# Performance work log

Hardware: AMD Instinct MI355X
Metric: run time of the kernel (lower is better)

## Reference

```python
import jax, jax.numpy as jnp
import numpy as np

B, TXT_T, MEL_T, N_MEL = 32, 256, 1600, 40
PAD_MAG = 1.0e12


def setup_inputs() -> dict:
    key = jax.random.key(0)
    k1, k2, k3, k4 = jax.random.split(key, 4)
    mu_logvar = jax.random.normal(k1, (B, TXT_T, 2 * N_MEL), jnp.float32)
    z = jax.random.normal(k2, (B, N_MEL, MEL_T), jnp.float32)
    text_lengths = jax.random.randint(k3, (B,), TXT_T // 2, TXT_T + 1).astype(jnp.int32)
    mel_lengths = jax.random.randint(k4, (B,), MEL_T // 2, MEL_T + 1).astype(jnp.int32)
    return {"mu_logvar": mu_logvar, "z": z,
            "text_lengths": text_lengths, "mel_lengths": mel_lengths}


def _mdn_log_prob(mu_logvar, z):
    # mu_logvar: [B, L, 2C], z: [B, C, T] -> log_prob_matrix [B, L, T]
    C = z.shape[1]
    mu, logvar = jnp.split(mu_logvar, 2, axis=-1)          # [B, L, C] each
    invvar = jnp.exp(-logvar)                               # [B, L, C]
    # mean_c((z - mu)^2 * invvar) expanded via matmuls (no [B,L,T,C] tensor)
    t1 = jnp.einsum('bct,blc->blt', z * z, invvar)
    t2 = jnp.einsum('bct,blc->blt', z, mu * invvar)
    t3 = jnp.sum(mu * mu * invvar, axis=-1)[:, :, None]
    mse = t1 - 2.0 * t2 + t3                                # [B, L, T]
    return -0.5 * (mse / C + jnp.mean(logvar, axis=-1)[:, :, None])


def _forward_dp(lp):
    # forward algorithm: log_alpha over (txt position, mel time) via scan over T
    Bb, L, T = lp.shape
    alpha0 = jnp.full((Bb, L + 1), -PAD_MAG, lp.dtype).at[:, 1].set(lp[:, 0, 0])

    def step(alpha, lp_t):
        stay = alpha[:, 1:] + 1e-7
        go = alpha[:, :-1] + 1e-7
        new = jnp.logaddexp(stay, go) + lp_t                # [B, L]
        alpha_new = jnp.concatenate(
            [jnp.full((Bb, 1), -PAD_MAG, lp.dtype), new], axis=1)
        return alpha_new, new

    _, ys = jax.lax.scan(step, alpha0, jnp.moveaxis(lp[:, :, 1:], 2, 0))
    log_alpha = jnp.concatenate([alpha0[:, 1:][None], ys], axis=0)  # [T, B, L]
    return log_alpha


def _viterbi(lp, text_lengths, mel_lengths):
    Bb, L, T = lp.shape
    beta0 = jnp.full((Bb, L), -PAD_MAG, lp.dtype).at[:, 0].set(lp[:, 0, 0])

    def fstep(beta, lp_t):
        shifted = jnp.concatenate(
            [jnp.full((Bb, 1), -PAD_MAG, lp.dtype), beta[:, :-1]], axis=1)
        new = jnp.maximum(beta, shifted) + lp_t
        return new, new

    _, ys = jax.lax.scan(fstep, beta0, jnp.moveaxis(lp[:, :, 1:], 2, 0))
    log_beta = jnp.transpose(jnp.concatenate([beta0[None], ys], axis=0), (1, 2, 0))  # [B, L, T]

    b_idx = jnp.arange(Bb)
    r0 = (text_lengths - 1).astype(jnp.float32)
    c0 = (mel_lengths - 1).astype(jnp.float32)

    def bstep(carry, _):
        rows, cols = carry
        ri = rows.astype(jnp.int32)
        ci = cols.astype(jnp.int32)
        # torch negative indexing wraps -> emulate with mod
        val_go = log_beta[b_idx, (ri - 1) % L, (ci - 1) % T]
        val_stay = log_beta[b_idx, ri % L, (ci - 1) % T]
        is_go = (val_go > val_stay).astype(rows.dtype)
        new_rows = jax.nn.relu(rows - is_go + 1.0) - 1.0
        new_cols = jax.nn.relu(cols) - 1.0
        return (new_rows, new_cols), new_rows

    _, path_ys = jax.lax.scan(bstep, (r0, c0), None, length=T - 1)
    full = jnp.concatenate([r0[None], path_ys], axis=0)     # [T, B], backward order
    path = full[::-1].T                                     # [B, T], chronological
    align = jax.nn.one_hot(path.astype(jnp.int32), L, dtype=lp.dtype)  # [B, T, L]

    def shift(a, ml):
        # F.pad(..., (-pad, pad)) on time axis: shift valid region to the front
        rolled = jnp.roll(a, -(T - ml), axis=0)
        mask = (jnp.arange(T) < ml)[:, None].astype(a.dtype)
        return rolled * mask

    return jax.vmap(shift)(align, mel_lengths)              # [B, T, L]


def reference(mu_logvar, z, text_lengths, mel_lengths):
    lp = _mdn_log_prob(mu_logvar, z)                        # [B, L, T]
    log_alpha = _forward_dp(lp)                             # [T, B, L]
    b_idx = jnp.arange(lp.shape[0])
    alpha_last = log_alpha[mel_lengths - 1, b_idx, text_lengths - 1]
    mdn_loss = -(alpha_last / mel_lengths.astype(alpha_last.dtype))  # [B]
    alignment = _viterbi(lp, text_lengths, mel_lengths)     # [B, T, L]
    return mdn_loss, alignment, lp
```

## Files before the change

### kernel.cpp

```cpp
#include <hip/hip_runtime.h>
#include <cstdint>
#include <math.h>

#define BB   32
#define LLEN 256
#define TLEN 1600
#define NC   40
#define NEGPADF (-1.0e12f)
#define NEGPADD (-1.0e12)
#define NBATCH 16
#define SUBB   8
#define NPROD  4
#define NBUF   2

#define LOG2E_F 1.4426950408889634f
#define LN2_F   0.6931471805599453f
#define C7F     1.4426950408889634e-7f

#define OFF_ALIGN 32
#define OFF_LP    (32 + (size_t)BB * TLEN * LLEN)

#define WSB_A    0
#define WSB_KC   (WSB_A + (size_t)BB * LLEN * 80 * 8)
#define WSB_LPT  (WSB_KC + (size_t)BB * LLEN * 8)

__device__ __forceinline__ int imin(int a, int b) { return a < b ? a : b; }

#define WAIT_LGKM0 0xC07F

__device__ __forceinline__ void bar_prod() {
  asm volatile("" ::: "memory");
  __builtin_amdgcn_s_waitcnt(WAIT_LGKM0);
  __builtin_amdgcn_s_barrier();
  asm volatile("" ::: "memory");
}
__device__ __forceinline__ void bar_cons() {
  asm volatile("" ::: "memory");
  __builtin_amdgcn_s_barrier();
  asm volatile("" ::: "memory");
}

__device__ __forceinline__ int rot1_i32(int x) {
  return __builtin_amdgcn_mov_dpp(x, 0x13C , 0xF, 0xF, true);
}
__device__ __forceinline__ float rot1_f32(float x) {
  return __int_as_float(rot1_i32(__float_as_int(x)));
}
__device__ __forceinline__ double rot1_f64(double x) {
  long long v = __double_as_longlong(x);
  int lo = rot1_i32((int)(v & 0xffffffffLL));
  int hi = rot1_i32((int)(v >> 32));
  return __longlong_as_double(((long long)hi << 32) | (unsigned long long)(unsigned int)lo);
}

__global__ __launch_bounds__(256) void prep_kernel(
    const float* __restrict__ mu_logvar, double* __restrict__ A, double* __restrict__ Kc) {
  int row = blockIdx.x * 4 + (threadIdx.x >> 6);
  int lane = threadIdx.x & 63;
  const float* src = mu_logvar + (size_t)row * (2 * NC);
  double mu = 0.0, lv = 0.0, iv = 0.0, part = 0.0;
  if (lane < NC) {
    mu = (double)src[lane];
    lv = (double)src[NC + lane];
    iv = exp(-lv);
    part = mu * mu * iv + lv;
  }
  for (int m = 1; m < 64; m <<= 1) part += __shfl_xor(part, m, 64);
  const double s = -0.5 / (double)NC;
  if (lane < NC) {
    A[(size_t)row * 80 + lane]      = s * iv;
    A[(size_t)row * 80 + NC + lane] = (1.0 / (double)NC) * mu * iv;
  }
  if (lane == 0) Kc[row] = s * part;
}

__global__ __launch_bounds__(128) void lp_kernel(
    const float* __restrict__ z, const double* __restrict__ A,
    const double* __restrict__ Kc, float* __restrict__ out,
    float* __restrict__ lpTh) {
  int b  = blockIdx.z;
  int l0 = blockIdx.y * 32;
  int t0 = blockIdx.x * 128;
  int tid = threadIdx.x;
  int t = t0 + tid;
  int tv = imin(t, TLEN - 1);
  bool act = (t < TLEN);

  float* lp_out = out + OFF_LP;
  float* loS    = out + OFF_ALIGN;

  float zr[NC];
  const float* zb = z + (size_t)b * NC * TLEN;
  #pragma unroll
  for (int c = 0; c < NC; ++c) zr[c] = zb[(size_t)c * TLEN + tv];

  __shared__ __align__(16) double tile[128][17];
  const double* Ab = A + ((size_t)b * LLEN + l0) * 80;
  const double* Kb = Kc + (size_t)b * LLEN + l0;

  for (int g = 0; g < 2; ++g) {
    for (int j16 = 0; j16 < 16; ++j16) {
      int j = g * 16 + j16;
      const double* Ar = Ab + (size_t)j * 80;
      double a0 = Kb[j], a1 = 0.0, a2 = 0.0, a3 = 0.0;
      #pragma unroll
      for (int c = 0; c < NC; c += 2) {
        double z0 = (double)zr[c], z1 = (double)zr[c + 1];
        a0 = fma(Ar[c],          z0 * z0, a0);
        a1 = fma(Ar[NC + c],     z0,      a1);
        a2 = fma(Ar[c + 1],      z1 * z1, a2);
        a3 = fma(Ar[NC + c + 1], z1,      a3);
      }
      double accd = (a0 + a2) + (a1 + a3);
      if (act) lp_out[((size_t)b * LLEN + l0 + j) * TLEN + t] = (float)accd;
      tile[tid][j16] = accd;
    }
    __syncthreads();
    #pragma unroll
    for (int p = 0; p < 4; ++p) {
      int idx = p * 128 + tid;
      int r = idx >> 2, c4 = idx & 3;
      int tr = t0 + r;
      if (tr < TLEN) {
        float h[4], lo[4];
        #pragma unroll
        for (int i = 0; i < 4; ++i) {
          double d = tile[r][c4 * 4 + i];
          float hh = (float)d;
          h[i] = hh;
          lo[i] = (float)(d - (double)hh);
        }
        size_t base = ((size_t)b * TLEN + tr) * LLEN + l0 + g * 16 + c4 * 4;
        *(float4*)(lpTh + base) = make_float4(h[0], h[1], h[2], h[3]);
        *(float4*)(loS + base)  = make_float4(lo[0], lo[1], lo[2], lo[3]);
      }
    }
    __syncthreads();
  }
}

__global__ __launch_bounds__(320, 1) void dp_kernel(
    const float* __restrict__ lpTh, const float* outR,
    const int* __restrict__ tlen, const int* __restrict__ mlen,
    float* __restrict__ out) {
  int bid = blockIdx.x;
  bool is_beta = (bid >= BB);
  int b = is_beta ? bid - BB : bid;
  int tid = threadIdx.x;
  int lane = tid & 63;
  int wv = tid >> 6;
  int tl = tlen[b];
  int ml = mlen[b];
  const float* lpb = lpTh + (size_t)b * TLEN * LLEN;
  const float* lob = outR + OFF_ALIGN + (size_t)b * TLEN * LLEN;
  float* al = out + OFF_ALIGN + (size_t)b * TLEN * LLEN;
  int nint = (ml - 2 + NBATCH) / NBATCH;

  __shared__ __align__(16) double bufd[NBUF][NBATCH][4][64];
  __shared__ uint32_t Dbits[LLEN][TLEN / 32];
  __shared__ int pathL[TLEN];
  float* bufaF = (float*)&bufd[0][0][0][0];

  if (wv >= 1) {
    int q = wv - 1;
    int nsb = 2 * nint;
    const float* ph = lpb + 4 * lane;
    const float* pl = lob + 4 * lane;
    float4 vh[SUBB], vl[SUBB];
    float4 z4 = make_float4(0.f, 0.f, 0.f, 0.f);
    auto issue = [&](int sb) {
      #pragma unroll
      for (int j = 0; j < SUBB; ++j) {
        int c = imin(1 + SUBB * sb + j, TLEN - 1);
        vh[j] = *(const float4*)(ph + (size_t)c * LLEN);
        if (is_beta) vl[j] = *(const float4*)(pl + (size_t)c * LLEN);
      }
    };
    auto store = [&](int sb) {
      int s  = (sb >> 1) % NBUF;
      int jb = (sb & 1) * SUBB;
      if (is_beta) {
        #pragma unroll
        for (int j = 0; j < SUBB; ++j) {
          bufd[s][jb + j][0][lane] = (double)vh[j].x + (double)vl[j].x;
          bufd[s][jb + j][1][lane] = (double)vh[j].y + (double)vl[j].y;
          bufd[s][jb + j][2][lane] = (double)vh[j].z + (double)vl[j].z;
          bufd[s][jb + j][3][lane] = (double)vh[j].w + (double)vl[j].w;
        }
      } else {
        #pragma unroll
        for (int j = 0; j < SUBB; ++j) {
          int off = ((s * NBATCH + jb + j) * 4) * 64 + lane;
          bufaF[off]       = fmaf(vh[j].x, LOG2E_F, C7F);
          bufaF[off + 64]  = fmaf(vh[j].y, LOG2E_F, C7F);
          bufaF[off + 128] = fmaf(vh[j].z, LOG2E_F, C7F);
          bufaF[off + 192] = fmaf(vh[j].w, LOG2E_F, C7F);
        }
      }
    };
    if (q < 2) {
      issue(q); store(q);
      if (q + NPROD < nsb) issue(q + NPROD);
    } else if (q < nsb) {
      issue(q);
    }
    for (int w = 0; w < nint; ++w) {
      bar_prod();
      int sb0 = 2 * w + 2;
      int mine = ((sb0 & 3) == q) ? sb0 : ((((sb0 + 1) & 3) == q) ? (sb0 + 1) : -1);
      if (mine >= 0 && mine < nsb) {
        store(mine);
        if (mine + NPROD < nsb) issue(mine + NPROD);
      }
      if (is_beta && w >= 1) {
        int zc = NBATCH * (w - 1) + 4 * q;
        float* az = al + (size_t)zc * LLEN + 4 * lane;
        #pragma unroll
        for (int k = 0; k < 4; ++k) *(float4*)(az + (size_t)k * LLEN) = z4;
      }
    }
    if (is_beta) {
      for (int c = NBATCH * (nint - 1) + q; c < TLEN; c += NPROD)
        *(float4*)(al + (size_t)c * LLEN + 4 * lane) = z4;
    }
  } else if (!is_beta) {
    float lp00 = lpb[0] * LOG2E_F;
    float o0 = (lane == 0) ? lp00 : NEGPADF;
    float o1 = NEGPADF, o2 = NEGPADF, o3 = NEGPADF;
    float f0 = o0, f1 = o1, f2 = o2, f3 = o3;
    float qv = rot1_f32(o3);
    int t = 1;
    for (int w = 0; w < nint; ++w) {
      bar_cons();
      int s = w % NBUF;
      #pragma unroll
      for (int j = 0; j < NBATCH; ++j, ++t) {
        int off = ((s * NBATCH + j) * 4) * 64 + lane;
        float l0 = bufaF[off];
        float l1 = bufaF[off + 64];
        float l2 = bufaF[off + 128];
        float l3 = bufaF[off + 192];
        float p = (lane == 0) ? NEGPADF : qv;
        float m0 = fmaxf(o0, p),  d0 = o0 - p;
        float m1 = fmaxf(o1, o0), d1 = o1 - o0;
        float m2 = fmaxf(o2, o1), d2 = o2 - o1;
        float m3 = fmaxf(o3, o2), d3 = o3 - o2;
        float n0 = m0 + __builtin_amdgcn_logf(1.0f + __builtin_amdgcn_exp2f(-fabsf(d0))) + l0;
        float n1 = m1 + __builtin_amdgcn_logf(1.0f + __builtin_amdgcn_exp2f(-fabsf(d1))) + l1;
        float n2 = m2 + __builtin_amdgcn_logf(1.0f + __builtin_amdgcn_exp2f(-fabsf(d2))) + l2;
        float n3 = m3 + __builtin_amdgcn_logf(1.0f + __builtin_amdgcn_exp2f(-fabsf(d3))) + l3;
        o0 = n0; o1 = n1; o2 = n2; o3 = n3;
        qv = rot1_f32(o3);
        if (t == ml - 1) { f0 = o0; f1 = o1; f2 = o2; f3 = o3; }
      }
    }
    int fr = tl - 1;
    if (lane == (fr >> 2)) {
      int sx = fr & 3;
      float val = (sx == 0) ? f0 : (sx == 1) ? f1 : (sx == 2) ? f2 : f3;
      out[b] = -val * LN2_F / (float)ml;
    }
  } else {
    double lp00 = (double)lpb[0] + (double)lob[0];
    double o0 = (lane == 0) ? lp00 : NEGPADD;
    double o1 = NEGPADD, o2 = NEGPADD, o3 = NEGPADD;
    uint32_t a0 = 0, a1 = (lane == 0) ? 1u : 0u, a2 = 0, a3 = 0;
    double qv = rot1_f64(o3);
    int t = 1;
    for (int w = 0; w < nint; ++w) {
      bar_cons();
      int s = w % NBUF;
      #pragma unroll
      for (int j = 0; j < NBATCH; ++j, ++t) {
        double l0 = bufd[s][j][0][lane];
        double l1 = bufd[s][j][1][lane];
        double l2 = bufd[s][j][2][lane];
        double l3 = bufd[s][j][3][lane];
        double p = (lane == 0) ? NEGPADD : qv;
        double n0 = fmax(o0, p)  + l0;
        double n1 = fmax(o1, o0) + l1;
        double n2 = fmax(o2, o1) + l2;
        double n3 = fmax(o3, o2) + l3;
        qv = rot1_f64(n3);
        uint32_t bit = 1u << (t & 31);
        if (qv > n0) a0 |= bit;
        if (n0 > n1) a1 |= bit;
        if (n1 > n2) a2 |= bit;
        if (n2 > n3) a3 |= bit;
        o0 = n0; o1 = n1; o2 = n2; o3 = n3;
        if ((t & 31) == 31) {
          int wd = t >> 5;
          Dbits[4 * lane + 0][wd] = a0; a0 = 0;
          Dbits[4 * lane + 1][wd] = a1; a1 = 0;
          Dbits[4 * lane + 2][wd] = a2; a2 = 0;
          Dbits[4 * lane + 3][wd] = a3; a3 = 0;
        }
      }
    }
    int tend = nint * NBATCH;
    int wd = tend >> 5;
    if ((tend & 31) != 31 && wd < TLEN / 32) {
      Dbits[4 * lane + 0][wd] = a0;
      Dbits[4 * lane + 1][wd] = a1;
      Dbits[4 * lane + 2][wd] = a2;
      Dbits[4 * lane + 3][wd] = a3;
    }
    __builtin_amdgcn_s_waitcnt(WAIT_LGKM0);

    if (lane == 0) {
      int r = tl - 1;
      pathL[ml - 1] = r;
      int curR = 1 << 30, curW = -1;
      uint32_t W = 0;
      for (int qq = ml - 2; qq >= 0; --qq) {
        int w2 = qq >> 5;
        if (r >= 0 && (r != curR || w2 != curW)) { W = Dbits[r][w2]; curR = r; curW = w2; }
        int g = (r >= 0) ? (int)((W >> (qq & 31)) & 1u) : 0;
        r -= g;
        pathL[qq] = r;
      }
    }
  }

  if (is_beta) {
    __syncthreads();
    for (int t = tid; t < ml; t += 320) {
      int p = pathL[t];
      if (p >= 0) al[(size_t)t * LLEN + p] = 1.0f;
    }
  }
}

extern "C" void kernel_launch(void* const* d_in, const int* in_sizes, int n_in,
                              void* d_out, int out_size, void* d_ws, size_t ws_size,
                              hipStream_t stream) {
  const float* mu_logvar = (const float*)d_in[0];
  const float* z         = (const float*)d_in[1];
  const int*   tlv       = (const int*)d_in[2];
  const int*   mlv       = (const int*)d_in[3];
  float* out = (float*)d_out;
  char*  wsb = (char*)d_ws;

  double* Ad   = (double*)(wsb + WSB_A);
  double* Kcd  = (double*)(wsb + WSB_KC);
  float*  lpTh = (float*)(wsb + WSB_LPT);

  prep_kernel<<<dim3(BB * LLEN / 4), 256, 0, stream>>>(mu_logvar, Ad, Kcd);
  lp_kernel<<<dim3(13, 8, BB), 128, 0, stream>>>(z, Ad, Kcd, out, lpTh);
  dp_kernel<<<dim3(2 * BB), 320, 0, stream>>>(lpTh, out, tlv, mlv, out);
}
```

Measured before the change: 516.0 us.

## Triple-buffer LDS staging and software-prefetch consumer loads four steps ahead

Raises the shared staging ring from two to three buffers and has producers fill one extra batch before the loop, so consumers can read into the next buffer early. Both the forward and Viterbi consumer loops now keep a 4-deep register ring of prefetched log-prob values, loading step j+4 while computing step j. This is meant to hide LDS load latency on the serial recurrence critical path. It costs more LDS and registers, especially in the f64 path, and needs an extra barrier so producer and consumer stay in lockstep.

```diff
diff --git a/kernel.cpp b/kernel.cpp
--- a/kernel.cpp
+++ b/kernel.cpp
@@ -11,7 +11,7 @@
 #define NBATCH 16
 #define SUBB   8
 #define NPROD  4
-#define NBUF   2
+#define NBUF   3
 
 #define LOG2E_F 1.4426950408889634f
 #define LN2_F   0.6931471805599453f
@@ -198,15 +198,14 @@
         }
       }
     };
-    if (q < 2) {
+    if (q < nsb) {
       issue(q); store(q);
       if (q + NPROD < nsb) issue(q + NPROD);
-    } else if (q < nsb) {
-      issue(q);
-    }
+    }
+    bar_prod();
     for (int w = 0; w < nint; ++w) {
       bar_prod();
-      int sb0 = 2 * w + 2;
+      int sb0 = 2 * w + 4;
       int mine = ((sb0 & 3) == q) ? sb0 : ((((sb0 + 1) & 3) == q) ? (sb0 + 1) : -1);
       if (mine >= 0 && mine < nsb) {
         store(mine);
@@ -229,17 +228,28 @@
     float o1 = NEGPADF, o2 = NEGPADF, o3 = NEGPADF;
     float f0 = o0, f1 = o1, f2 = o2, f3 = o3;
     float qv = rot1_f32(o3);
+    bar_cons();
+    float P[4][4];
+    #pragma unroll
+    for (int i = 0; i < 4; ++i) {
+      const float* src = bufaF + i * 256;
+      P[i][0] = src[lane]; P[i][1] = src[64 + lane];
+      P[i][2] = src[128 + lane]; P[i][3] = src[192 + lane];
+    }
     int t = 1;
     for (int w = 0; w < nint; ++w) {
       bar_cons();
-      int s = w % NBUF;
+      int s = w % NBUF, sn = (w + 1) % NBUF;
+      const float* baseS = bufaF + s * (NBATCH * 256);
+      const float* baseN = bufaF + sn * (NBATCH * 256);
       #pragma unroll
       for (int j = 0; j < NBATCH; ++j, ++t) {
-        int off = ((s * NBATCH + j) * 4) * 64 + lane;
-        float l0 = bufaF[off];
-        float l1 = bufaF[off + 64];
-        float l2 = bufaF[off + 128];
-        float l3 = bufaF[off + 192];
+        int rj = j & 3;
+        float l0 = P[rj][0], l1 = P[rj][1], l2 = P[rj][2], l3 = P[rj][3];
+        const float* src = (j < NBATCH - 4) ? (baseS + (j + 4) * 256)
+                                            : (baseN + (j + 4 - NBATCH) * 256);
+        P[rj][0] = src[lane];       P[rj][1] = src[64 + lane];
+        P[rj][2] = src[128 + lane]; P[rj][3] = src[192 + lane];
         float p = (lane == 0) ? NEGPADF : qv;
         float m0 = fmaxf(o0, p),  d0 = o0 - p;
         float m1 = fmaxf(o1, o0), d1 = o1 - o0;
@@ -266,16 +276,28 @@
     double o1 = NEGPADD, o2 = NEGPADD, o3 = NEGPADD;
     uint32_t a0 = 0, a1 = (lane == 0) ? 1u : 0u, a2 = 0, a3 = 0;
     double qv = rot1_f64(o3);
+    bar_cons();
+    double P[4][4];
+    #pragma unroll
+    for (int i = 0; i < 4; ++i) {
+      P[i][0] = bufd[0][i][0][lane]; P[i][1] = bufd[0][i][1][lane];
+      P[i][2] = bufd[0][i][2][lane]; P[i][3] = bufd[0][i][3][lane];
+    }
     int t = 1;
     for (int w = 0; w < nint; ++w) {
       bar_cons();
-      int s = w % NBUF;
+      int s = w % NBUF, sn = (w + 1) % NBUF;
+      const double (*bs)[4][64] = bufd[s];
+      const double (*bn)[4][64] = bufd[sn];
       #pragma unroll
       for (int j = 0; j < NBATCH; ++j, ++t) {
-        double l0 = bufd[s][j][0][lane];
-        double l1 = bufd[s][j][1][lane];
-        double l2 = bufd[s][j][2][lane];
-        double l3 = bufd[s][j][3][lane];
+        int rj = j & 3;
+        double l0 = P[rj][0], l1 = P[rj][1], l2 = P[rj][2], l3 = P[rj][3];
+        {
+          const double (*src)[64] = (j < NBATCH - 4) ? bs[j + 4] : bn[j + 4 - NBATCH];
+          P[rj][0] = src[0][lane]; P[rj][1] = src[1][lane];
+          P[rj][2] = src[2][lane]; P[rj][3] = src[3][lane];
+        }
         double p = (lane == 0) ? NEGPADD : qv;
         double n0 = fmax(o0, p)  + l0;
         double n1 = fmax(o1, o0) + l1;
```

New measurement: 489.6 us. 1.05x faster.

## Replace producer-wave LDS pipeline with single-wave register prefetch in DP kernel

Applied to the files above, without the earlier changes.

The DP kernel drops its four producer wavefronts, the double-buffered LDS staging and the per-batch block barriers. Each block is now one wavefront that prefetches the log-prob columns eight steps ahead into registers with a rotating set of float4 loads, and it zeroes the alignment rows inline. This removes barrier and LDS round-trip cost from the serial recurrence. The loop now runs over all TLEN steps instead of stopping at the mel length, and global load latency is hidden only by the eight-step prefetch depth.

```diff
diff --git a/kernel.cpp b/kernel.cpp
--- a/kernel.cpp
+++ b/kernel.cpp
@@ -8,10 +8,6 @@
 #define NC   40
 #define NEGPADF (-1.0e12f)
 #define NEGPADD (-1.0e12)
-#define NBATCH 16
-#define SUBB   8
-#define NPROD  4
-#define NBUF   2
 
 #define LOG2E_F 1.4426950408889634f
 #define LN2_F   0.6931471805599453f
@@ -27,18 +23,7 @@
 __device__ __forceinline__ int imin(int a, int b) { return a < b ? a : b; }
 
 #define WAIT_LGKM0 0xC07F
-
-__device__ __forceinline__ void bar_prod() {
-  asm volatile("" ::: "memory");
-  __builtin_amdgcn_s_waitcnt(WAIT_LGKM0);
-  __builtin_amdgcn_s_barrier();
-  asm volatile("" ::: "memory");
-}
-__device__ __forceinline__ void bar_cons() {
-  asm volatile("" ::: "memory");
-  __builtin_amdgcn_s_barrier();
-  asm volatile("" ::: "memory");
-}
+#define WAIT_VM0   0x3F70
 
 __device__ __forceinline__ int rot1_i32(int x) {
   return __builtin_amdgcn_mov_dpp(x, 0x13C , 0xF, 0xF, true);
@@ -139,120 +124,65 @@
   }
 }
 
-__global__ __launch_bounds__(320, 1) void dp_kernel(
+__global__ __launch_bounds__(64, 1) void dp_kernel(
     const float* __restrict__ lpTh, const float* outR,
     const int* __restrict__ tlen, const int* __restrict__ mlen,
-    float* __restrict__ out) {
+    float* out) {
   int bid = blockIdx.x;
   bool is_beta = (bid >= BB);
   int b = is_beta ? bid - BB : bid;
-  int tid = threadIdx.x;
-  int lane = tid & 63;
-  int wv = tid >> 6;
+  int lane = threadIdx.x & 63;
   int tl = tlen[b];
   int ml = mlen[b];
   const float* lpb = lpTh + (size_t)b * TLEN * LLEN;
   const float* lob = outR + OFF_ALIGN + (size_t)b * TLEN * LLEN;
   float* al = out + OFF_ALIGN + (size_t)b * TLEN * LLEN;
-  int nint = (ml - 2 + NBATCH) / NBATCH;
-
-  __shared__ __align__(16) double bufd[NBUF][NBATCH][4][64];
+
   __shared__ uint32_t Dbits[LLEN][TLEN / 32];
   __shared__ int pathL[TLEN];
-  float* bufaF = (float*)&bufd[0][0][0][0];
-
-  if (wv >= 1) {
-    int q = wv - 1;
-    int nsb = 2 * nint;
-    const float* ph = lpb + 4 * lane;
-    const float* pl = lob + 4 * lane;
-    float4 vh[SUBB], vl[SUBB];
-    float4 z4 = make_float4(0.f, 0.f, 0.f, 0.f);
-    auto issue = [&](int sb) {
-      #pragma unroll
-      for (int j = 0; j < SUBB; ++j) {
-        int c = imin(1 + SUBB * sb + j, TLEN - 1);
-        vh[j] = *(const float4*)(ph + (size_t)c * LLEN);
-        if (is_beta) vl[j] = *(const float4*)(pl + (size_t)c * LLEN);
-      }
-    };
-    auto store = [&](int sb) {
-      int s  = (sb >> 1) % NBUF;
-      int jb = (sb & 1) * SUBB;
-      if (is_beta) {
-        #pragma unroll
-        for (int j = 0; j < SUBB; ++j) {
-          bufd[s][jb + j][0][lane] = (double)vh[j].x + (double)vl[j].x;
-          bufd[s][jb + j][1][lane] = (double)vh[j].y + (double)vl[j].y;
-          bufd[s][jb + j][2][lane] = (double)vh[j].z + (double)vl[j].z;
-          bufd[s][jb + j][3][lane] = (double)vh[j].w + (double)vl[j].w;
-        }
-      } else {
-        #pragma unroll
-        for (int j = 0; j < SUBB; ++j) {
-          int off = ((s * NBATCH + jb + j) * 4) * 64 + lane;
-          bufaF[off]       = fmaf(vh[j].x, LOG2E_F, C7F);
-          bufaF[off + 64]  = fmaf(vh[j].y, LOG2E_F, C7F);
-          bufaF[off + 128] = fmaf(vh[j].z, LOG2E_F, C7F);
-          bufaF[off + 192] = fmaf(vh[j].w, LOG2E_F, C7F);
-        }
-      }
-    };
-    if (q < 2) {
-      issue(q); store(q);
-      if (q + NPROD < nsb) issue(q + NPROD);
-    } else if (q < nsb) {
-      issue(q);
-    }
-    for (int w = 0; w < nint; ++w) {
-      bar_prod();
-      int sb0 = 2 * w + 2;
-      int mine = ((sb0 & 3) == q) ? sb0 : ((((sb0 + 1) & 3) == q) ? (sb0 + 1) : -1);
-      if (mine >= 0 && mine < nsb) {
-        store(mine);
-        if (mine + NPROD < nsb) issue(mine + NPROD);
-      }
-      if (is_beta && w >= 1) {
-        int zc = NBATCH * (w - 1) + 4 * q;
-        float* az = al + (size_t)zc * LLEN + 4 * lane;
-        #pragma unroll
-        for (int k = 0; k < 4; ++k) *(float4*)(az + (size_t)k * LLEN) = z4;
-      }
-    }
-    if (is_beta) {
-      for (int c = NBATCH * (nint - 1) + q; c < TLEN; c += NPROD)
-        *(float4*)(al + (size_t)c * LLEN + 4 * lane) = z4;
-    }
-  } else if (!is_beta) {
+
+  const float* ph = lpb + 4 * lane;
+
+  if (!is_beta) {
     float lp00 = lpb[0] * LOG2E_F;
     float o0 = (lane == 0) ? lp00 : NEGPADF;
     float o1 = NEGPADF, o2 = NEGPADF, o3 = NEGPADF;
     float f0 = o0, f1 = o1, f2 = o2, f3 = o3;
     float qv = rot1_f32(o3);
+    float4 h0 = *(const float4*)(ph + 1 * LLEN);
+    float4 h1 = *(const float4*)(ph + 2 * LLEN);
+    float4 h2 = *(const float4*)(ph + 3 * LLEN);
+    float4 h3 = *(const float4*)(ph + 4 * LLEN);
+    float4 h4 = *(const float4*)(ph + 5 * LLEN);
+    float4 h5 = *(const float4*)(ph + 6 * LLEN);
+    float4 h6 = *(const float4*)(ph + 7 * LLEN);
+    float4 h7 = *(const float4*)(ph + 8 * LLEN);
     int t = 1;
-    for (int w = 0; w < nint; ++w) {
-      bar_cons();
-      int s = w % NBUF;
-      #pragma unroll
-      for (int j = 0; j < NBATCH; ++j, ++t) {
-        int off = ((s * NBATCH + j) * 4) * 64 + lane;
-        float l0 = bufaF[off];
-        float l1 = bufaF[off + 64];
-        float l2 = bufaF[off + 128];
-        float l3 = bufaF[off + 192];
-        float p = (lane == 0) ? NEGPADF : qv;
-        float m0 = fmaxf(o0, p),  d0 = o0 - p;
-        float m1 = fmaxf(o1, o0), d1 = o1 - o0;
-        float m2 = fmaxf(o2, o1), d2 = o2 - o1;
-        float m3 = fmaxf(o3, o2), d3 = o3 - o2;
-        float n0 = m0 + __builtin_amdgcn_logf(1.0f + __builtin_amdgcn_exp2f(-fabsf(d0))) + l0;
-        float n1 = m1 + __builtin_amdgcn_logf(1.0f + __builtin_amdgcn_exp2f(-fabsf(d1))) + l1;
-        float n2 = m2 + __builtin_amdgcn_logf(1.0f + __builtin_amdgcn_exp2f(-fabsf(d2))) + l2;
-        float n3 = m3 + __builtin_amdgcn_logf(1.0f + __builtin_amdgcn_exp2f(-fabsf(d3))) + l3;
-        o0 = n0; o1 = n1; o2 = n2; o3 = n3;
-        qv = rot1_f32(o3);
-        if (t == ml - 1) { f0 = o0; f1 = o1; f2 = o2; f3 = o3; }
-      }
+    auto stepA = [&](float4& hs) {
+      float4 hv = hs;
+      int c = imin(t + 8, TLEN - 1);
+      hs = *(const float4*)(ph + (size_t)c * LLEN);
+      float l0 = fmaf(hv.x, LOG2E_F, C7F);
+      float l1 = fmaf(hv.y, LOG2E_F, C7F);
+      float l2 = fmaf(hv.z, LOG2E_F, C7F);
+      float l3 = fmaf(hv.w, LOG2E_F, C7F);
+      float p = (lane == 0) ? NEGPADF : qv;
+      float m0 = fmaxf(o0, p),  d0 = o0 - p;
+      float m1 = fmaxf(o1, o0), d1 = o1 - o0;
+      float m2 = fmaxf(o2, o1), d2 = o2 - o1;
+      float m3 = fmaxf(o3, o2), d3 = o3 - o2;
+      float n0 = m0 + __builtin_amdgcn_logf(1.0f + __builtin_amdgcn_exp2f(-fabsf(d0))) + l0;
+      float n1 = m1 + __builtin_amdgcn_logf(1.0f + __builtin_amdgcn_exp2f(-fabsf(d1))) + l1;
+      float n2 = m2 + __builtin_amdgcn_logf(1.0f + __builtin_amdgcn_exp2f(-fabsf(d2))) + l2;
+      float n3 = m3 + __builtin_amdgcn_logf(1.0f + __builtin_amdgcn_exp2f(-fabsf(d3))) + l3;
+      o0 = n0; o1 = n1; o2 = n2; o3 = n3;
+      qv = rot1_f32(o3);
+      if (t == ml - 1) { f0 = o0; f1 = o1; f2 = o2; f3 = o3; }
+      ++t;
+    };
+    for (int tb = 0; tb < TLEN / 8; ++tb) {
+      stepA(h0); stepA(h1); stepA(h2); stepA(h3);
+      stepA(h4); stepA(h5); stepA(h6); stepA(h7);
     }
     int fr = tl - 1;
     if (lane == (fr >> 2)) {
@@ -260,74 +190,87 @@
       float val = (sx == 0) ? f0 : (sx == 1) ? f1 : (sx == 2) ? f2 : f3;
       out[b] = -val * LN2_F / (float)ml;
     }
-  } else {
-    double lp00 = (double)lpb[0] + (double)lob[0];
-    double o0 = (lane == 0) ? lp00 : NEGPADD;
-    double o1 = NEGPADD, o2 = NEGPADD, o3 = NEGPADD;
-    uint32_t a0 = 0, a1 = (lane == 0) ? 1u : 0u, a2 = 0, a3 = 0;
-    double qv = rot1_f64(o3);
-    int t = 1;
-    for (int w = 0; w < nint; ++w) {
-      bar_cons();
-      int s = w % NBUF;
-      #pragma unroll
-      for (int j = 0; j < NBATCH; ++j, ++t) {
-        double l0 = bufd[s][j][0][lane];
-        double l1 = bufd[s][j][1][lane];
-        double l2 = bufd[s][j][2][lane];
-        double l3 = bufd[s][j][3][lane];
-        double p = (lane == 0) ? NEGPADD : qv;
-        double n0 = fmax(o0, p)  + l0;
-        double n1 = fmax(o1, o0) + l1;
-        double n2 = fmax(o2, o1) + l2;
-        double n3 = fmax(o3, o2) + l3;
-        qv = rot1_f64(n3);
-        uint32_t bit = 1u << (t & 31);
-        if (qv > n0) a0 |= bit;
-        if (n0 > n1) a1 |= bit;
-        if (n1 > n2) a2 |= bit;
-        if (n2 > n3) a3 |= bit;
-        o0 = n0; o1 = n1; o2 = n2; o3 = n3;
-        if ((t & 31) == 31) {
-          int wd = t >> 5;
-          Dbits[4 * lane + 0][wd] = a0; a0 = 0;
-          Dbits[4 * lane + 1][wd] = a1; a1 = 0;
-          Dbits[4 * lane + 2][wd] = a2; a2 = 0;
-          Dbits[4 * lane + 3][wd] = a3; a3 = 0;
-        }
-      }
-    }
-    int tend = nint * NBATCH;
-    int wd = tend >> 5;
-    if ((tend & 31) != 31 && wd < TLEN / 32) {
-      Dbits[4 * lane + 0][wd] = a0;
-      Dbits[4 * lane + 1][wd] = a1;
-      Dbits[4 * lane + 2][wd] = a2;
-      Dbits[4 * lane + 3][wd] = a3;
-    }
-    __builtin_amdgcn_s_waitcnt(WAIT_LGKM0);
-
-    if (lane == 0) {
-      int r = tl - 1;
-      pathL[ml - 1] = r;
-      int curR = 1 << 30, curW = -1;
-      uint32_t W = 0;
-      for (int qq = ml - 2; qq >= 0; --qq) {
-        int w2 = qq >> 5;
-        if (r >= 0 && (r != curR || w2 != curW)) { W = Dbits[r][w2]; curR = r; curW = w2; }
-        int g = (r >= 0) ? (int)((W >> (qq & 31)) & 1u) : 0;
-        r -= g;
-        pathL[qq] = r;
-      }
-    }
-  }
-
-  if (is_beta) {
-    __syncthreads();
-    for (int t = tid; t < ml; t += 320) {
-      int p = pathL[t];
-      if (p >= 0) al[(size_t)t * LLEN + p] = 1.0f;
-    }
+    return;
+  }
+
+  const float* pl = lob + 4 * lane;
+  float* az = al + 4 * lane;
+  float4 z4 = make_float4(0.f, 0.f, 0.f, 0.f);
+  double lp00 = (double)lpb[0] + (double)lob[0];
+  double o0 = (lane == 0) ? lp00 : NEGPADD;
+  double o1 = NEGPADD, o2 = NEGPADD, o3 = NEGPADD;
+  uint32_t a0 = 0, a1 = (lane == 0) ? 1u : 0u, a2 = 0, a3 = 0;
+  double qv = rot1_f64(o3);
+  float4 h0 = *(const float4*)(ph + 1 * LLEN), g0 = *(const float4*)(pl + 1 * LLEN);
+  float4 h1 = *(const float4*)(ph + 2 * LLEN), g1 = *(const float4*)(pl + 2 * LLEN);
+  float4 h2 = *(const float4*)(ph + 3 * LLEN), g2 = *(const float4*)(pl + 3 * LLEN);
+  float4 h3 = *(const float4*)(ph + 4 * LLEN), g3 = *(const float4*)(pl + 4 * LLEN);
+  float4 h4 = *(const float4*)(ph + 5 * LLEN), g4 = *(const float4*)(pl + 5 * LLEN);
+  float4 h5 = *(const float4*)(ph + 6 * LLEN), g5 = *(const float4*)(pl + 6 * LLEN);
+  float4 h6 = *(const float4*)(ph + 7 * LLEN), g6 = *(const float4*)(pl + 7 * LLEN);
+  float4 h7 = *(const float4*)(ph + 8 * LLEN), g7 = *(const float4*)(pl + 8 * LLEN);
+  int t = 1;
+  auto stepB = [&](float4& hs, float4& gs) {
+    float4 hv = hs; float4 gv = gs;
+    int c = imin(t + 8, TLEN - 1);
+    hs = *(const float4*)(ph + (size_t)c * LLEN);
+    gs = *(const float4*)(pl + (size_t)c * LLEN);
+    double l0 = (double)hv.x + (double)gv.x;
+    double l1 = (double)hv.y + (double)gv.y;
+    double l2 = (double)hv.z + (double)gv.z;
+    double l3 = (double)hv.w + (double)gv.w;
+    double p = (lane == 0) ? NEGPADD : qv;
+    double n0 = fmax(o0, p)  + l0;
+    double n1 = fmax(o1, o0) + l1;
+    double n2 = fmax(o2, o1) + l2;
+    double n3 = fmax(o3, o2) + l3;
+    qv = rot1_f64(n3);
+    uint32_t bit = 1u << (t & 31);
+    if (qv > n0) a0 |= bit;
+    if (n0 > n1) a1 |= bit;
+    if (n1 > n2) a2 |= bit;
+    if (n2 > n3) a3 |= bit;
+    o0 = n0; o1 = n1; o2 = n2; o3 = n3;
+    if ((t & 31) == 31) {
+      int wd = t >> 5;
+      Dbits[4 * lane + 0][wd] = a0; a0 = 0;
+      Dbits[4 * lane + 1][wd] = a1; a1 = 0;
+      Dbits[4 * lane + 2][wd] = a2; a2 = 0;
+      Dbits[4 * lane + 3][wd] = a3; a3 = 0;
+    }
+    if (t > 8) *(float4*)(az + (size_t)(t - 8) * LLEN) = z4;
+    ++t;
+  };
+  for (int tb = 0; tb < TLEN / 8; ++tb) {
+    stepB(h0, g0); stepB(h1, g1); stepB(h2, g2); stepB(h3, g3);
+    stepB(h4, g4); stepB(h5, g5); stepB(h6, g6); stepB(h7, g7);
+  }
+  *(float4*)az = z4;
+  #pragma unroll
+  for (int c = TLEN - 7; c < TLEN; ++c)
+    *(float4*)(az + (size_t)c * LLEN) = z4;
+
+  __builtin_amdgcn_s_waitcnt(WAIT_LGKM0);
+
+  if (lane == 0) {
+    int r = tl - 1;
+    pathL[ml - 1] = r;
+    int curR = 1 << 30, curW = -1;
+    uint32_t W = 0;
+    for (int qq = ml - 2; qq >= 0; --qq) {
+      int w2 = qq >> 5;
+      if (r >= 0 && (r != curR || w2 != curW)) { W = Dbits[r][w2]; curR = r; curW = w2; }
+      int g = (r >= 0) ? (int)((W >> (qq & 31)) & 1u) : 0;
+      r -= g;
+      pathL[qq] = r;
+    }
+  }
+  __builtin_amdgcn_s_waitcnt(WAIT_LGKM0);
+  __builtin_amdgcn_s_waitcnt(WAIT_VM0);
+
+  for (int tt = lane; tt < ml; tt += 64) {
+    int p = pathL[tt];
+    if (p >= 0) al[(size_t)tt * LLEN + p] = 1.0f;
   }
 }
 
@@ -347,5 +290,5 @@
 
   prep_kernel<<<dim3(BB * LLEN / 4), 256, 0, stream>>>(mu_logvar, Ad, Kcd);
   lp_kernel<<<dim3(13, 8, BB), 128, 0, stream>>>(z, Ad, Kcd, out, lpTh);
-  dp_kernel<<<dim3(2 * BB), 320, 0, stream>>>(lpTh, out, tlv, mlv, out);
-}
+  dp_kernel<<<dim3(2 * BB), 64, 0, stream>>>(lpTh, out, tlv, mlv, out);
+}
```

Measured after the change: 549.9 us. +6.6%, slower.
